# Kernel optimization log

Hardware: AMD Instinct MI355X
Metric: run time of the kernel (lower is better)

The kernel has to match this reference:

```python
import jax, jax.numpy as jnp
import numpy as np

K = 4
EPS = 1e-6
NEG_INF = -1e9


def _extract_patches(x, k):
    # x: [C, H, W] -> [P, C*k*k], P = (H-k+1)*(W-k+1), p = hp*Wp + wp
    C, H, W = x.shape
    Hp, Wp = H - k + 1, W - k + 1
    cols = jnp.stack([x[:, di:di + Hp, dj:dj + Wp]
                      for di in range(k) for dj in range(k)], axis=1)  # [C, k*k, Hp, Wp]
    return cols.reshape(C * k * k, Hp * Wp).T  # [P, C*k*k]


def setup_inputs() -> dict:
    key = jax.random.key(0)
    k1, k2, k3 = jax.random.split(key, 3)
    C, H, W = 32, 80, 80
    low = jax.random.normal(k1, (1, C, H, W), dtype=jnp.float32)
    high = jax.random.normal(k2, (1, C, H, W), dtype=jnp.float32)
    mask = jax.random.randint(k3, (H + 1, W + 1), 0, 2, dtype=jnp.int32)
    return {"low_level_features": low, "hight_level_features": high, "mask": mask}


def reference(low_level_features, hight_level_features, mask):
    k = K
    low = low_level_features[0]    # [C, H, W]
    high = hight_level_features[0]
    C, H, W = low.shape
    Hp, Wp = H - k + 1, W - k + 1
    P = Hp * Wp

    low_p = _extract_patches(low, k)    # [P, D], D = C*k*k (candidate patches)
    high_p = _extract_patches(high, k)  # [P, D] (query filters)
    norms = jnp.sqrt(jnp.sum(low_p * low_p, axis=1))  # torch.norm per patch, [P]

    # all-pairs cosine-distance scores: [P_query, P_candidate]
    scores = jnp.einsum('qd,pd->qp', high_p, low_p) / (norms + EPS)[None, :]
    # candidates where mask==1 (top-left of patch) are excluded (set to inf=-1e9)
    excl = (mask[:Hp, :Wp].reshape(-1) == 1)
    scores = jnp.where(excl[None, :], NEG_INF, scores)
    best = jnp.argmax(scores, axis=1)   # [P] best match per query patch

    # a query patch at (i,j) is processed only if its 4 mask corners are nonzero
    valid = ((mask[:Hp, :Wp] != 0) & (mask[:Hp, k:k + Wp] != 0) &
             (mask[k:k + Hp, :Wp] != 0) & (mask[k:k + Hp, k:k + Wp] != 0))
    validf = valid.astype(low.dtype).reshape(-1)  # [P]

    gathered = low_p[best] * validf[:, None]            # [P, D]
    g = gathered.reshape(Hp, Wp, C, k, k)               # per-query result patches
    vmap2d = validf.reshape(Hp, Wp)

    result = jnp.zeros_like(low)
    counts = jnp.zeros((H, W), low.dtype)
    for di in range(k):
        for dj in range(k):
            result = result.at[:, di:di + Hp, dj:dj + Wp].add(
                jnp.moveaxis(g[:, :, :, di, dj], -1, 0))
            counts = counts.at[di:di + Hp, dj:dj + Wp].add(vmap2d)

    out = result / (counts + EPS)[None, :, :]
    nz = counts != 0
    out = out * nz[None, :, :] + low * (~nz)[None, :, :]
    return out[None]  # [1, C, H, W]
```

## Files before the change

### kernel.cpp

```cpp
#include <hip/hip_runtime.h>
#include <hip/hip_bf16.h>

#define CC    32
#define HH    80
#define WW    80
#define HW    6400
#define HPQ   77
#define WPQ   77
#define PP    5929
#define DD    512
#define MSTR  81
#define NTILE 93
#define QTILES 372
#define NEGINF (-1e9f)

typedef __attribute__((ext_vector_type(4))) float f32x4;
typedef __attribute__((ext_vector_type(8))) short bf16x8;
typedef __attribute__((ext_vector_type(8))) unsigned short u16x8;

__device__ __forceinline__ void split_bf16(float v, unsigned short& hi, unsigned short& lo) {
    __hip_bfloat16 h = __float2bfloat16(v);
    float hf = __bfloat162float(h);
    __hip_bfloat16 lw = __float2bfloat16(v - hf);
    hi = *reinterpret_cast<unsigned short*>(&h);
    lo = *reinterpret_cast<unsigned short*>(&lw);
}

__global__ __launch_bounds__(256) void k_flags(const float* __restrict__ low,
                                               const int* __restrict__ mask,
                                               float* __restrict__ invn,
                                               int* __restrict__ excl,
                                               int* __restrict__ valid,
                                               int* __restrict__ qlist,
                                               int* __restrict__ nvalid) {
    __shared__ float part[4][64];
    const int tid = threadIdx.x;
    const int pl = tid & 63;
    const int sl = tid >> 6;
    const int p = blockIdx.x * 64 + pl;

    float s = 0.f;
    if (p < PP) {
        int pi = p / WPQ, pj = p % WPQ;
        int base = pi * WW + pj;
        for (int c = sl * 8; c < sl * 8 + 8; ++c) {
            int b2 = c * HW + base;
#pragma unroll
            for (int di = 0; di < 4; ++di)
#pragma unroll
                for (int dj = 0; dj < 4; ++dj) {
                    float v = low[b2 + di * WW + dj];
                    s += v * v;
                }
        }
    }
    part[sl][pl] = s;
    __syncthreads();
    if (tid < 64 && p < PP) {
        float t = part[0][tid] + part[1][tid] + part[2][tid] + part[3][tid];
        invn[p] = 1.0f / (sqrtf(t) + 1e-6f);
        int pi = p / WPQ, pj = p % WPQ;
        int m00 = mask[pi * MSTR + pj];
        int m01 = mask[pi * MSTR + pj + 4];
        int m10 = mask[(pi + 4) * MSTR + pj];
        int m11 = mask[(pi + 4) * MSTR + pj + 4];
        excl[p] = (m00 == 1) ? 1 : 0;
        int v = (m00 != 0 && m01 != 0 && m10 != 0 && m11 != 0) ? 1 : 0;
        valid[p] = v;
        if (v) {
            int slot = atomicAdd(nvalid, 1);
            qlist[slot] = p;
        }
    }
}

__global__ __launch_bounds__(256) void k_packB(const float* __restrict__ low,
                                               const float* __restrict__ invn,
                                               unsigned short* __restrict__ Bhi,
                                               unsigned short* __restrict__ Blo) {
    int t = blockIdx.x * 256 + threadIdx.x;
    if (t >= QTILES * 16 * 64) return;
    int l = t & 63;
    int s = (t >> 6) & 15;
    int u = t >> 10;
    int n = l & 15, quad = l >> 4;
    int p = u * 16 + n;
    int kbase = s * 32 + quad * 8;

    u16x8 vh, vl;
    if (p < PP) {
        float sc = invn[p];
        int pi = p / WPQ, pj = p % WPQ;
        int base = (kbase >> 4) * HW + pi * WW + pj;
#pragma unroll
        for (int j = 0; j < 8; ++j) {
            int kk = kbase + j;
            int di = (kk >> 2) & 3, dj = kk & 3;
            float v = low[base + di * WW + dj] * sc;
            unsigned short h, lo;
            split_bf16(v, h, lo);
            vh[j] = h; vl[j] = lo;
        }
    } else {
#pragma unroll
        for (int j = 0; j < 8; ++j) { vh[j] = 0; vl[j] = 0; }
    }
    int off = t * 8;
    *reinterpret_cast<u16x8*>(Bhi + off) = vh;
    *reinterpret_cast<u16x8*>(Blo + off) = vl;
}

__global__ __launch_bounds__(256) void k_packA(const float* __restrict__ high,
                                               const int* __restrict__ qlist,
                                               const int* __restrict__ nvalid,
                                               unsigned short* __restrict__ Ahi,
                                               unsigned short* __restrict__ Alo) {
    int t = blockIdx.x * 256 + threadIdx.x;
    if (t >= QTILES * 16 * 64) return;
    int nv = *nvalid;
    int l = t & 63;
    int s = (t >> 6) & 15;
    int u = t >> 10;
    if ((u >> 2) * 64 >= nv) return;
    int m = l & 15, quad = l >> 4;
    int slot = u * 16 + m;
    int kbase = s * 32 + quad * 8;

    u16x8 vh, vl;
    if (slot < nv) {
        int q = qlist[slot];
        int qi = q / WPQ, qj = q % WPQ;
        int base = (kbase >> 4) * HW + qi * WW + qj;
#pragma unroll
        for (int j = 0; j < 8; ++j) {
            int kk = kbase + j;
            int di = (kk >> 2) & 3, dj = kk & 3;
            float v = high[base + di * WW + dj];
            unsigned short h, lo;
            split_bf16(v, h, lo);
            vh[j] = h; vl[j] = lo;
        }
    } else {
#pragma unroll
        for (int j = 0; j < 8; ++j) { vh[j] = 0; vl[j] = 0; }
    }
    int off = t * 8;
    *reinterpret_cast<u16x8*>(Ahi + off) = vh;
    *reinterpret_cast<u16x8*>(Alo + off) = vl;
}

__global__ __launch_bounds__(256) void k_score(const unsigned short* __restrict__ Ahi,
                                               const unsigned short* __restrict__ Alo,
                                               const unsigned short* __restrict__ Bhi,
                                               const unsigned short* __restrict__ Blo,
                                               const int* __restrict__ excl,
                                               const int* __restrict__ nvalid,
                                               float* __restrict__ pscore,
                                               int* __restrict__ pidx) {
    const int nv = *nvalid;
    const int qblk = blockIdx.y;
    if (qblk * 64 >= nv) return;
    const int pblk = blockIdx.x;
    const int w = threadIdx.x >> 6;
    const int l = threadIdx.x & 63;
    const int qtile = qblk * 4 + w;

    f32x4 acc[4];
#pragma unroll
    for (int pt = 0; pt < 4; ++pt) acc[pt] = (f32x4){0.f, 0.f, 0.f, 0.f};

    const int abase = qtile * 8192 + l * 8;
    const int bbase0 = pblk * 4 * 8192 + l * 8;

#pragma unroll 4
    for (int s = 0; s < 16; ++s) {
        bf16x8 ah = *reinterpret_cast<const bf16x8*>(Ahi + abase + s * 512);
        bf16x8 al = *reinterpret_cast<const bf16x8*>(Alo + abase + s * 512);
#pragma unroll
        for (int pt = 0; pt < 4; ++pt) {
            int boff = bbase0 + pt * 8192 + s * 512;
            bf16x8 bh = *reinterpret_cast<const bf16x8*>(Bhi + boff);
            bf16x8 bl = *reinterpret_cast<const bf16x8*>(Blo + boff);
            acc[pt] = __builtin_amdgcn_mfma_f32_16x16x32_bf16(ah, bh, acc[pt], 0, 0, 0);
            acc[pt] = __builtin_amdgcn_mfma_f32_16x16x32_bf16(ah, bl, acc[pt], 0, 0, 0);
            acc[pt] = __builtin_amdgcn_mfma_f32_16x16x32_bf16(al, bh, acc[pt], 0, 0, 0);
        }
    }

    const int n = l & 15, quad = l >> 4;
    float bs[4]; int bi[4];
#pragma unroll
    for (int r = 0; r < 4; ++r) { bs[r] = -3.4e38f; bi[r] = 0x7fffffff; }
#pragma unroll
    for (int pt = 0; pt < 4; ++pt) {
        int gp = pblk * 64 + pt * 16 + n;
        if (gp < PP) {
            bool ex = (excl[gp] != 0);
#pragma unroll
            for (int r = 0; r < 4; ++r) {
                float sv = ex ? NEGINF : acc[pt][r];
                if (sv > bs[r]) { bs[r] = sv; bi[r] = gp; }
            }
        }
    }
#pragma unroll
    for (int off = 1; off <= 8; off <<= 1) {
#pragma unroll
        for (int r = 0; r < 4; ++r) {
            float s2 = __shfl_xor(bs[r], off, 64);
            int   i2 = __shfl_xor(bi[r], off, 64);
            if (s2 > bs[r] || (s2 == bs[r] && i2 < bi[r])) { bs[r] = s2; bi[r] = i2; }
        }
    }
    if (n == 0) {
#pragma unroll
        for (int r = 0; r < 4; ++r) {
            int slot = qtile * 16 + quad * 4 + r;
            pscore[slot * NTILE + pblk] = bs[r];
            pidx[slot * NTILE + pblk] = bi[r];
        }
    }
}

__global__ __launch_bounds__(64) void k_reduce(const float* __restrict__ pscore,
                                               const int* __restrict__ pidx,
                                               const int* __restrict__ qlist,
                                               const int* __restrict__ nvalid,
                                               int* __restrict__ best) {
    const int slot = blockIdx.x;
    if (slot >= *nvalid) return;
    const int t = threadIdx.x;
    float bs = -3.4e38f;
    int bi = 0x7fffffff;
    for (int k = t; k < NTILE; k += 64) {
        float s = pscore[slot * NTILE + k];
        int i = pidx[slot * NTILE + k];
        if (s > bs || (s == bs && i < bi)) { bs = s; bi = i; }
    }
#pragma unroll
    for (int off = 32; off >= 1; off >>= 1) {
        float s2 = __shfl_down(bs, off);
        int   i2 = __shfl_down(bi, off);
        if (s2 > bs || (s2 == bs && i2 < bi)) { bs = s2; bi = i2; }
    }
    if (t == 0) best[qlist[slot]] = bi;
}

__global__ __launch_bounds__(256) void k_prep(const int* __restrict__ best,
                                              const int* __restrict__ valid,
                                              int* __restrict__ cnt,
                                              int* __restrict__ offlist) {
    int pix = blockIdx.x * 256 + threadIdx.x;
    if (pix >= HW) return;
    int i = pix / WW, j = pix % WW;
    int n = 0;
#pragma unroll
    for (int di = 0; di < 4; ++di) {
        int qi = i - di;
        if (qi < 0 || qi >= HPQ) continue;
#pragma unroll
        for (int dj = 0; dj < 4; ++dj) {
            int qj = j - dj;
            if (qj < 0 || qj >= WPQ) continue;
            int q = qi * WPQ + qj;
            if (valid[q]) {
                int b = best[q];
                int bi = b / WPQ, bj = b % WPQ;
                offlist[pix * 16 + n] = (bi + di) * WW + (bj + dj);
                n++;
            }
        }
    }
    cnt[pix] = n;
}

__global__ __launch_bounds__(256) void k_out(const float* __restrict__ low,
                                             const int* __restrict__ cnt,
                                             const int* __restrict__ offlist,
                                             float* __restrict__ out) {
    int idx = blockIdx.x * 256 + threadIdx.x;
    if (idx >= CC * HW) return;
    int c = idx / HW;
    int pix = idx % HW;
    int n = cnt[pix];
    if (n > 0) {
        int base = c * HW;
        float acc = 0.f;
        for (int t = 0; t < n; ++t)
            acc += low[base + offlist[pix * 16 + t]];
        out[idx] = acc / ((float)n + 1e-6f);
    } else {
        out[idx] = low[idx];
    }
}

extern "C" void kernel_launch(void* const* d_in, const int* in_sizes, int n_in,
                              void* d_out, int out_size, void* d_ws, size_t ws_size,
                              hipStream_t stream) {
    const float* low  = (const float*)d_in[0];
    const float* high = (const float*)d_in[1];
    const int*   mask = (const int*)d_in[2];
    float* out = (float*)d_out;

    char* ws = (char*)d_ws;
    int*   nvalid = (int*)(ws);
    int*   qlist  = (int*)(ws + 64);
    float* invn   = (float*)(ws + 24064);
    int*   excl   = (int*)(ws + 48128);
    int*   valid  = (int*)(ws + 72192);
    int*   best   = (int*)(ws + 96256);
    float* pscore = (float*)(ws + 120320);
    int*   pidx   = (int*)(ws + 2334464);
    int*   cnt    = (int*)(ws + 4548608);
    int*   offlist= (int*)(ws + 4574208);
    unsigned short* Ahi = (unsigned short*)(ws + 4983808);
    unsigned short* Alo = (unsigned short*)(ws + 11078656);
    unsigned short* Bhi = (unsigned short*)(ws + 17173504);
    unsigned short* Blo = (unsigned short*)(ws + 23268352);

    hipMemsetAsync(nvalid, 0, 4, stream);
    hipLaunchKernelGGL(k_flags, dim3((PP + 63) / 64), dim3(256), 0, stream,
                       low, mask, invn, excl, valid, qlist, nvalid);
    hipLaunchKernelGGL(k_packB, dim3(QTILES * 4), dim3(256), 0, stream,
                       low, invn, Bhi, Blo);
    hipLaunchKernelGGL(k_packA, dim3(QTILES * 4), dim3(256), 0, stream,
                       high, qlist, nvalid, Ahi, Alo);
    hipLaunchKernelGGL(k_score, dim3(NTILE, 93), dim3(256), 0, stream,
                       Ahi, Alo, Bhi, Blo, excl, nvalid, pscore, pidx);
    hipLaunchKernelGGL(k_reduce, dim3(5952), dim3(64), 0, stream,
                       pscore, pidx, qlist, nvalid, best);
    hipLaunchKernelGGL(k_prep, dim3((HW + 255) / 256), dim3(256), 0, stream,
                       best, valid, cnt, offlist);
    hipLaunchKernelGGL(k_out, dim3((CC * HW + 255) / 256), dim3(256), 0, stream,
                       low, cnt, offlist, out);
}
```

Measured before the change: 111.1 us.

## Fuse pipeline into four kernels with atomic packed argmax and register-tiled scoring

Merges the A and B pack kernels into one launch. The score kernel now computes a 4x4 tile grid per wave over a persistent query-block loop and folds the argmax in directly through a 64-bit packed atomicMax, which removes the partial-score buffers and the separate reduce kernel. The prep and output kernels are also fused, with the per-pixel offset list built in shared memory. The goal is fewer launches, less global traffic and more reuse of the A/B fragments per load. In exchange it adds atomic contention, higher register pressure from 16 accumulators, and a smaller grid for the score kernel.

```diff
diff --git a/kernel.cpp b/kernel.cpp
--- a/kernel.cpp
+++ b/kernel.cpp
@@ -30,7 +30,7 @@
                                                const int* __restrict__ mask,
                                                float* __restrict__ invn,
                                                int* __restrict__ excl,
-                                               int* __restrict__ valid,
+                                               int* __restrict__ qslot,
                                                int* __restrict__ qlist,
                                                int* __restrict__ nvalid) {
     __shared__ float part[4][64];
@@ -66,87 +66,86 @@
         int m11 = mask[(pi + 4) * MSTR + pj + 4];
         excl[p] = (m00 == 1) ? 1 : 0;
         int v = (m00 != 0 && m01 != 0 && m10 != 0 && m11 != 0) ? 1 : 0;
-        valid[p] = v;
+        int slot = -1;
         if (v) {
-            int slot = atomicAdd(nvalid, 1);
+            slot = atomicAdd(nvalid, 1);
             qlist[slot] = p;
         }
-    }
-}
-
-__global__ __launch_bounds__(256) void k_packB(const float* __restrict__ low,
-                                               const float* __restrict__ invn,
-                                               unsigned short* __restrict__ Bhi,
-                                               unsigned short* __restrict__ Blo) {
-    int t = blockIdx.x * 256 + threadIdx.x;
-    if (t >= QTILES * 16 * 64) return;
-    int l = t & 63;
-    int s = (t >> 6) & 15;
-    int u = t >> 10;
-    int n = l & 15, quad = l >> 4;
-    int p = u * 16 + n;
-    int kbase = s * 32 + quad * 8;
-
-    u16x8 vh, vl;
-    if (p < PP) {
-        float sc = invn[p];
-        int pi = p / WPQ, pj = p % WPQ;
-        int base = (kbase >> 4) * HW + pi * WW + pj;
-#pragma unroll
-        for (int j = 0; j < 8; ++j) {
-            int kk = kbase + j;
-            int di = (kk >> 2) & 3, dj = kk & 3;
-            float v = low[base + di * WW + dj] * sc;
-            unsigned short h, lo;
-            split_bf16(v, h, lo);
-            vh[j] = h; vl[j] = lo;
-        }
+        qslot[p] = slot;
+    }
+}
+
+__global__ __launch_bounds__(256) void k_pack(const float* __restrict__ low,
+                                              const float* __restrict__ high,
+                                              const float* __restrict__ invn,
+                                              const int* __restrict__ qlist,
+                                              const int* __restrict__ nvalid,
+                                              unsigned short* __restrict__ Bhi,
+                                              unsigned short* __restrict__ Blo,
+                                              unsigned short* __restrict__ Ahi,
+                                              unsigned short* __restrict__ Alo) {
+    const int g = blockIdx.x;
+    if (g < QTILES * 4) {
+        int t = g * 256 + threadIdx.x;
+        int l = t & 63;
+        int s = (t >> 6) & 15;
+        int u = t >> 10;
+        int n = l & 15, quad = l >> 4;
+        int p = u * 16 + n;
+        int kbase = s * 32 + quad * 8;
+        u16x8 vh, vl;
+        if (p < PP) {
+            float sc = invn[p];
+            int pi = p / WPQ, pj = p % WPQ;
+            int base = (kbase >> 4) * HW + pi * WW + pj;
+#pragma unroll
+            for (int j = 0; j < 8; ++j) {
+                int kk = kbase + j;
+                int di = (kk >> 2) & 3, dj = kk & 3;
+                float v = low[base + di * WW + dj] * sc;
+                unsigned short h, lo;
+                split_bf16(v, h, lo);
+                vh[j] = h; vl[j] = lo;
+            }
+        } else {
+#pragma unroll
+            for (int j = 0; j < 8; ++j) { vh[j] = 0; vl[j] = 0; }
+        }
+        int off = t * 8;
+        *reinterpret_cast<u16x8*>(Bhi + off) = vh;
+        *reinterpret_cast<u16x8*>(Blo + off) = vl;
     } else {
-#pragma unroll
-        for (int j = 0; j < 8; ++j) { vh[j] = 0; vl[j] = 0; }
-    }
-    int off = t * 8;
-    *reinterpret_cast<u16x8*>(Bhi + off) = vh;
-    *reinterpret_cast<u16x8*>(Blo + off) = vl;
-}
-
-__global__ __launch_bounds__(256) void k_packA(const float* __restrict__ high,
-                                               const int* __restrict__ qlist,
-                                               const int* __restrict__ nvalid,
-                                               unsigned short* __restrict__ Ahi,
-                                               unsigned short* __restrict__ Alo) {
-    int t = blockIdx.x * 256 + threadIdx.x;
-    if (t >= QTILES * 16 * 64) return;
-    int nv = *nvalid;
-    int l = t & 63;
-    int s = (t >> 6) & 15;
-    int u = t >> 10;
-    if ((u >> 2) * 64 >= nv) return;
-    int m = l & 15, quad = l >> 4;
-    int slot = u * 16 + m;
-    int kbase = s * 32 + quad * 8;
-
-    u16x8 vh, vl;
-    if (slot < nv) {
-        int q = qlist[slot];
-        int qi = q / WPQ, qj = q % WPQ;
-        int base = (kbase >> 4) * HW + qi * WW + qj;
-#pragma unroll
-        for (int j = 0; j < 8; ++j) {
-            int kk = kbase + j;
-            int di = (kk >> 2) & 3, dj = kk & 3;
-            float v = high[base + di * WW + dj];
-            unsigned short h, lo;
-            split_bf16(v, h, lo);
-            vh[j] = h; vl[j] = lo;
-        }
-    } else {
-#pragma unroll
-        for (int j = 0; j < 8; ++j) { vh[j] = 0; vl[j] = 0; }
-    }
-    int off = t * 8;
-    *reinterpret_cast<u16x8*>(Ahi + off) = vh;
-    *reinterpret_cast<u16x8*>(Alo + off) = vl;
+        int t = (g - QTILES * 4) * 256 + threadIdx.x;
+        int nv = *nvalid;
+        int l = t & 63;
+        int s = (t >> 6) & 15;
+        int u = t >> 10;
+        if ((u >> 2) * 64 >= nv) return;
+        int m = l & 15, quad = l >> 4;
+        int slot = u * 16 + m;
+        int kbase = s * 32 + quad * 8;
+        u16x8 vh, vl;
+        if (slot < nv) {
+            int q = qlist[slot];
+            int qi = q / WPQ, qj = q % WPQ;
+            int base = (kbase >> 4) * HW + qi * WW + qj;
+#pragma unroll
+            for (int j = 0; j < 8; ++j) {
+                int kk = kbase + j;
+                int di = (kk >> 2) & 3, dj = kk & 3;
+                float v = high[base + di * WW + dj];
+                unsigned short h, lo;
+                split_bf16(v, h, lo);
+                vh[j] = h; vl[j] = lo;
+            }
+        } else {
+#pragma unroll
+            for (int j = 0; j < 8; ++j) { vh[j] = 0; vl[j] = 0; }
+        }
+        int off = t * 8;
+        *reinterpret_cast<u16x8*>(Ahi + off) = vh;
+        *reinterpret_cast<u16x8*>(Alo + off) = vl;
+    }
 }
 
 __global__ __launch_bounds__(256) void k_score(const unsigned short* __restrict__ Ahi,
@@ -155,142 +154,138 @@
                                                const unsigned short* __restrict__ Blo,
                                                const int* __restrict__ excl,
                                                const int* __restrict__ nvalid,
-                                               float* __restrict__ pscore,
-                                               int* __restrict__ pidx) {
+                                               unsigned long long* __restrict__ bestpk) {
     const int nv = *nvalid;
-    const int qblk = blockIdx.y;
-    if (qblk * 64 >= nv) return;
-    const int pblk = blockIdx.x;
     const int w = threadIdx.x >> 6;
     const int l = threadIdx.x & 63;
-    const int qtile = qblk * 4 + w;
-
-    f32x4 acc[4];
-#pragma unroll
-    for (int pt = 0; pt < 4; ++pt) acc[pt] = (f32x4){0.f, 0.f, 0.f, 0.f};
-
-    const int abase = qtile * 8192 + l * 8;
-    const int bbase0 = pblk * 4 * 8192 + l * 8;
-
-#pragma unroll 4
-    for (int s = 0; s < 16; ++s) {
-        bf16x8 ah = *reinterpret_cast<const bf16x8*>(Ahi + abase + s * 512);
-        bf16x8 al = *reinterpret_cast<const bf16x8*>(Alo + abase + s * 512);
-#pragma unroll
-        for (int pt = 0; pt < 4; ++pt) {
-            int boff = bbase0 + pt * 8192 + s * 512;
-            bf16x8 bh = *reinterpret_cast<const bf16x8*>(Bhi + boff);
-            bf16x8 bl = *reinterpret_cast<const bf16x8*>(Blo + boff);
-            acc[pt] = __builtin_amdgcn_mfma_f32_16x16x32_bf16(ah, bh, acc[pt], 0, 0, 0);
-            acc[pt] = __builtin_amdgcn_mfma_f32_16x16x32_bf16(ah, bl, acc[pt], 0, 0, 0);
-            acc[pt] = __builtin_amdgcn_mfma_f32_16x16x32_bf16(al, bh, acc[pt], 0, 0, 0);
-        }
-    }
-
+    const int pblk = blockIdx.x * 4 + w;
     const int n = l & 15, quad = l >> 4;
-    float bs[4]; int bi[4];
-#pragma unroll
-    for (int r = 0; r < 4; ++r) { bs[r] = -3.4e38f; bi[r] = 0x7fffffff; }
+    const int bbase = pblk * 4 * 8192 + l * 8;
+
+    int gpv[4]; bool exv[4];
 #pragma unroll
     for (int pt = 0; pt < 4; ++pt) {
-        int gp = pblk * 64 + pt * 16 + n;
-        if (gp < PP) {
-            bool ex = (excl[gp] != 0);
-#pragma unroll
-            for (int r = 0; r < 4; ++r) {
-                float sv = ex ? NEGINF : acc[pt][r];
-                if (sv > bs[r]) { bs[r] = sv; bi[r] = gp; }
-            }
-        }
-    }
-#pragma unroll
-    for (int off = 1; off <= 8; off <<= 1) {
-#pragma unroll
-        for (int r = 0; r < 4; ++r) {
-            float s2 = __shfl_xor(bs[r], off, 64);
-            int   i2 = __shfl_xor(bi[r], off, 64);
-            if (s2 > bs[r] || (s2 == bs[r] && i2 < bi[r])) { bs[r] = s2; bi[r] = i2; }
-        }
-    }
-    if (n == 0) {
-#pragma unroll
-        for (int r = 0; r < 4; ++r) {
-            int slot = qtile * 16 + quad * 4 + r;
-            pscore[slot * NTILE + pblk] = bs[r];
-            pidx[slot * NTILE + pblk] = bi[r];
-        }
-    }
-}
-
-__global__ __launch_bounds__(64) void k_reduce(const float* __restrict__ pscore,
-                                               const int* __restrict__ pidx,
-                                               const int* __restrict__ qlist,
-                                               const int* __restrict__ nvalid,
-                                               int* __restrict__ best) {
-    const int slot = blockIdx.x;
-    if (slot >= *nvalid) return;
-    const int t = threadIdx.x;
-    float bs = -3.4e38f;
-    int bi = 0x7fffffff;
-    for (int k = t; k < NTILE; k += 64) {
-        float s = pscore[slot * NTILE + k];
-        int i = pidx[slot * NTILE + k];
-        if (s > bs || (s == bs && i < bi)) { bs = s; bi = i; }
-    }
-#pragma unroll
-    for (int off = 32; off >= 1; off >>= 1) {
-        float s2 = __shfl_down(bs, off);
-        int   i2 = __shfl_down(bi, off);
-        if (s2 > bs || (s2 == bs && i2 < bi)) { bs = s2; bi = i2; }
-    }
-    if (t == 0) best[qlist[slot]] = bi;
-}
-
-__global__ __launch_bounds__(256) void k_prep(const int* __restrict__ best,
-                                              const int* __restrict__ valid,
-                                              int* __restrict__ cnt,
-                                              int* __restrict__ offlist) {
-    int pix = blockIdx.x * 256 + threadIdx.x;
-    if (pix >= HW) return;
-    int i = pix / WW, j = pix % WW;
-    int n = 0;
-#pragma unroll
-    for (int di = 0; di < 4; ++di) {
-        int qi = i - di;
-        if (qi < 0 || qi >= HPQ) continue;
-#pragma unroll
-        for (int dj = 0; dj < 4; ++dj) {
-            int qj = j - dj;
-            if (qj < 0 || qj >= WPQ) continue;
-            int q = qi * WPQ + qj;
-            if (valid[q]) {
-                int b = best[q];
-                int bi = b / WPQ, bj = b % WPQ;
-                offlist[pix * 16 + n] = (bi + di) * WW + (bj + dj);
-                n++;
-            }
-        }
-    }
-    cnt[pix] = n;
+        gpv[pt] = pblk * 64 + pt * 16 + n;
+        exv[pt] = (gpv[pt] < PP) ? (excl[gpv[pt]] != 0) : true;
+    }
+
+    for (int qblk = blockIdx.y; qblk * 64 < nv; qblk += 12) {
+        f32x4 acc[4][4];
+#pragma unroll
+        for (int qt = 0; qt < 4; ++qt)
+#pragma unroll
+            for (int pt = 0; pt < 4; ++pt) acc[qt][pt] = (f32x4){0.f, 0.f, 0.f, 0.f};
+
+        const int abase = qblk * 4 * 8192 + l * 8;
+#pragma unroll 2
+        for (int s = 0; s < 16; ++s) {
+            bf16x8 ah[4], al[4];
+#pragma unroll
+            for (int qt = 0; qt < 4; ++qt) {
+                ah[qt] = *reinterpret_cast<const bf16x8*>(Ahi + abase + qt * 8192 + s * 512);
+                al[qt] = *reinterpret_cast<const bf16x8*>(Alo + abase + qt * 8192 + s * 512);
+            }
+#pragma unroll
+            for (int pt = 0; pt < 4; ++pt) {
+                bf16x8 bh = *reinterpret_cast<const bf16x8*>(Bhi + bbase + pt * 8192 + s * 512);
+                bf16x8 bl = *reinterpret_cast<const bf16x8*>(Blo + bbase + pt * 8192 + s * 512);
+#pragma unroll
+                for (int qt = 0; qt < 4; ++qt) {
+                    acc[qt][pt] = __builtin_amdgcn_mfma_f32_16x16x32_bf16(ah[qt], bh, acc[qt][pt], 0, 0, 0);
+                    acc[qt][pt] = __builtin_amdgcn_mfma_f32_16x16x32_bf16(ah[qt], bl, acc[qt][pt], 0, 0, 0);
+                    acc[qt][pt] = __builtin_amdgcn_mfma_f32_16x16x32_bf16(al[qt], bh, acc[qt][pt], 0, 0, 0);
+                }
+            }
+        }
+
+#pragma unroll
+        for (int qt = 0; qt < 4; ++qt) {
+            float bs[4]; int bi[4];
+#pragma unroll
+            for (int r = 0; r < 4; ++r) { bs[r] = -3.4e38f; bi[r] = 0x7fffffff; }
+#pragma unroll
+            for (int pt = 0; pt < 4; ++pt) {
+                if (gpv[pt] < PP) {
+#pragma unroll
+                    for (int r = 0; r < 4; ++r) {
+                        float sv = exv[pt] ? NEGINF : acc[qt][pt][r];
+                        if (sv > bs[r]) { bs[r] = sv; bi[r] = gpv[pt]; }
+                    }
+                }
+            }
+#pragma unroll
+            for (int off = 1; off <= 8; off <<= 1) {
+#pragma unroll
+                for (int r = 0; r < 4; ++r) {
+                    float s2 = __shfl_xor(bs[r], off, 64);
+                    int   i2 = __shfl_xor(bi[r], off, 64);
+                    if (s2 > bs[r] || (s2 == bs[r] && i2 < bi[r])) { bs[r] = s2; bi[r] = i2; }
+                }
+            }
+            if (n == 0) {
+#pragma unroll
+                for (int r = 0; r < 4; ++r) {
+                    if (bi[r] != 0x7fffffff) {
+                        unsigned ub = __float_as_uint(bs[r]);
+                        unsigned mo = (ub & 0x80000000u) ? ~ub : (ub | 0x80000000u);
+                        unsigned long long pk =
+                            ((unsigned long long)mo << 32) | (unsigned)(~bi[r]);
+                        int slot = (qblk * 4 + qt) * 16 + quad * 4 + r;
+                        atomicMax(bestpk + slot, pk);
+                    }
+                }
+            }
+        }
+    }
 }
 
 __global__ __launch_bounds__(256) void k_out(const float* __restrict__ low,
-                                             const int* __restrict__ cnt,
-                                             const int* __restrict__ offlist,
+                                             const int* __restrict__ qslot,
+                                             const unsigned long long* __restrict__ bestpk,
                                              float* __restrict__ out) {
-    int idx = blockIdx.x * 256 + threadIdx.x;
-    if (idx >= CC * HW) return;
-    int c = idx / HW;
-    int pix = idx % HW;
-    int n = cnt[pix];
-    if (n > 0) {
+    __shared__ int scnt[64];
+    __shared__ int soff[64][17];
+    const int tid = threadIdx.x;
+    const int pixb = blockIdx.x * 64;
+    if (tid < 64) {
+        int pix = pixb + tid;
+        int i = pix / WW, j = pix % WW;
+        int nn = 0;
+#pragma unroll
+        for (int di = 0; di < 4; ++di) {
+            int qi = i - di;
+            if (qi < 0 || qi >= HPQ) continue;
+#pragma unroll
+            for (int dj = 0; dj < 4; ++dj) {
+                int qj = j - dj;
+                if (qj < 0 || qj >= WPQ) continue;
+                int sl = qslot[qi * WPQ + qj];
+                if (sl >= 0) {
+                    int b = (int)(~(unsigned)bestpk[sl]);
+                    soff[tid][nn++] = (b / WPQ + di) * WW + (b % WPQ + dj);
+                }
+            }
+        }
+        scnt[tid] = nn;
+    }
+    __syncthreads();
+    const int pl = tid & 63, cg = tid >> 6;
+    const int nn = scnt[pl];
+    const int pix = pixb + pl;
+    const float inv = 1.0f / ((float)nn + 1e-6f);
+#pragma unroll
+    for (int k = 0; k < 8; ++k) {
+        int c = cg * 8 + k;
         int base = c * HW;
-        float acc = 0.f;
-        for (int t = 0; t < n; ++t)
-            acc += low[base + offlist[pix * 16 + t]];
-        out[idx] = acc / ((float)n + 1e-6f);
-    } else {
-        out[idx] = low[idx];
+        float a;
+        if (nn > 0) {
+            a = 0.f;
+            for (int t2 = 0; t2 < nn; ++t2) a += low[base + soff[pl][t2]];
+            a *= inv;
+        } else {
+            a = low[base + pix];
+        }
+        out[base + pix] = a;
     }
 }
 
@@ -303,34 +298,24 @@
     float* out = (float*)d_out;
 
     char* ws = (char*)d_ws;
-    int*   nvalid = (int*)(ws);
-    int*   qlist  = (int*)(ws + 64);
-    float* invn   = (float*)(ws + 24064);
-    int*   excl   = (int*)(ws + 48128);
-    int*   valid  = (int*)(ws + 72192);
-    int*   best   = (int*)(ws + 96256);
-    float* pscore = (float*)(ws + 120320);
-    int*   pidx   = (int*)(ws + 2334464);
-    int*   cnt    = (int*)(ws + 4548608);
-    int*   offlist= (int*)(ws + 4574208);
-    unsigned short* Ahi = (unsigned short*)(ws + 4983808);
-    unsigned short* Alo = (unsigned short*)(ws + 11078656);
-    unsigned short* Bhi = (unsigned short*)(ws + 17173504);
-    unsigned short* Blo = (unsigned short*)(ws + 23268352);
-
-    hipMemsetAsync(nvalid, 0, 4, stream);
-    hipLaunchKernelGGL(k_flags, dim3((PP + 63) / 64), dim3(256), 0, stream,
-                       low, mask, invn, excl, valid, qlist, nvalid);
-    hipLaunchKernelGGL(k_packB, dim3(QTILES * 4), dim3(256), 0, stream,
-                       low, invn, Bhi, Blo);
-    hipLaunchKernelGGL(k_packA, dim3(QTILES * 4), dim3(256), 0, stream,
-                       high, qlist, nvalid, Ahi, Alo);
-    hipLaunchKernelGGL(k_score, dim3(NTILE, 93), dim3(256), 0, stream,
-                       Ahi, Alo, Bhi, Blo, excl, nvalid, pscore, pidx);
-    hipLaunchKernelGGL(k_reduce, dim3(5952), dim3(64), 0, stream,
-                       pscore, pidx, qlist, nvalid, best);
-    hipLaunchKernelGGL(k_prep, dim3((HW + 255) / 256), dim3(256), 0, stream,
-                       best, valid, cnt, offlist);
-    hipLaunchKernelGGL(k_out, dim3((CC * HW + 255) / 256), dim3(256), 0, stream,
-                       low, cnt, offlist, out);
-}
+    int* nvalid = (int*)ws;
+    unsigned long long* bestpk = (unsigned long long*)(ws + 64);
+    int*   qlist = (int*)(ws + 49216);
+    int*   qslot = (int*)(ws + 73024);
+    float* invn  = (float*)(ws + 96832);
+    int*   excl  = (int*)(ws + 120640);
+    unsigned short* Ahi = (unsigned short*)(ws + 144448);
+    unsigned short* Alo = (unsigned short*)(ws + 6239296);
+    unsigned short* Bhi = (unsigned short*)(ws + 12334144);
+    unsigned short* Blo = (unsigned short*)(ws + 18625600);
+
+    hipMemsetAsync(ws, 0, 49216, stream);
+    hipLaunchKernelGGL(k_flags, dim3(NTILE), dim3(256), 0, stream,
+                       low, mask, invn, excl, qslot, qlist, nvalid);
+    hipLaunchKernelGGL(k_pack, dim3(QTILES * 8), dim3(256), 0, stream,
+                       low, high, invn, qlist, nvalid, Bhi, Blo, Ahi, Alo);
+    hipLaunchKernelGGL(k_score, dim3(24, 12), dim3(256), 0, stream,
+                       Ahi, Alo, Bhi, Blo, excl, nvalid, bestpk);
+    hipLaunchKernelGGL(k_out, dim3(100), dim3(256), 0, stream,
+                       low, qslot, bestpk, out);
+}
```

Result: slower. 114.2 us (+2.8%).
